# Kernel optimization log

Measured on AMD Instinct MI355X. Metric: run time of the kernel, lower is better.

Reference implementation:

```python
import jax, jax.numpy as jnp
import numpy as np

N = 100_000   # nodes
E = 600_000   # edges
D = 128       # embed_dim
G = 1000      # graphs (batch ids)
L = 3         # num_layers


def setup_inputs() -> dict:
    key = jax.random.key(0)
    ks = jax.random.split(key, 12)
    s = 1.0 / np.sqrt(D)
    return {
        "x": jax.random.normal(ks[0], (N, D), jnp.float32),
        "edge_index": jax.random.randint(ks[1], (2, E), 0, N),
        "batch": jnp.sort(jax.random.randint(ks[2], (N,), 0, G)),
        "mask": jax.random.randint(ks[3], (N,), 0, 2),
        # stacked GCNConv weights/biases (in=hidden=out=D)
        "gcn_w": jax.random.normal(ks[4], (L, D, D), jnp.float32) * s,
        "gcn_b": jnp.zeros((L, D), jnp.float32),
        # MLP head: Linear(D,D) -> ReLU -> Linear(D,1)
        "lin1_w": jax.random.normal(ks[5], (D, D), jnp.float32) * s,
        "lin1_b": jnp.zeros((D,), jnp.float32),
        "lin2_w": jax.random.normal(ks[6], (D,), jnp.float32) * s,
        "lin2_b": jnp.zeros((), jnp.float32),
    }


def gcn_forward(x, src, dst, gcn_w, gcn_b):
    # symmetric gcn_norm with self-loops: deg[i] = 1 + in-degree(i)
    deg = jax.ops.segment_sum(jnp.ones((E,), x.dtype), dst, num_segments=N) + 1.0
    dinv = jax.lax.rsqrt(deg)
    enorm = dinv[src] * dinv[dst]          # [E] edge normalization
    self_norm = (dinv * dinv)[:, None]     # [N,1] self-loop normalization
    h = x
    for l in range(L):
        h = h @ gcn_w[l]                   # [N,D]
        h = (jax.ops.segment_sum(h[src] * enorm[:, None], dst, num_segments=N)
             + h * self_norm)
        h = h + gcn_b[l]
        if l < L - 1:
            h = jax.nn.relu(h)  # (dropout inactive at inference)
    return h


def reference(x, edge_index, batch, mask, gcn_w, gcn_b, lin1_w, lin1_b, lin2_w, lin2_b):
    src, dst = edge_index[0], edge_index[1]
    h = gcn_forward(x, src, dst, gcn_w, gcn_b)
    # MLP head -> per-node score [N]
    s = jax.nn.relu(h @ lin1_w + lin1_b) @ lin2_w + lin2_b
    s = jnp.where(mask == 0, jnp.float32(-1e9), s)
    # per-graph (segment) softmax — fused replacement for the unique/batch loop
    m = jax.ops.segment_max(s, batch, num_segments=G)
    e = jnp.exp(s - m[batch])
    z = jax.ops.segment_sum(e, batch, num_segments=G)
    return e / z[batch]
```

## Files before the change

### kernel.cpp

```cpp
#include <hip/hip_runtime.h>
#include <hip/hip_bf16.h>
#include <stdint.h>

typedef unsigned int u32;
typedef unsigned short u16;
typedef __attribute__((ext_vector_type(8))) short bf16x8;
typedef __attribute__((ext_vector_type(4))) float f32x4;

__device__ __forceinline__ float u16tof(u16 u){ return __uint_as_float(((u32)u) << 16); }
__device__ __forceinline__ float lo16(u32 v){ return __uint_as_float(v << 16); }
__device__ __forceinline__ float hi16(u32 v){ return __uint_as_float(v & 0xffff0000u); }
__device__ __forceinline__ u16 ftobf(float f){
  u32 b = __float_as_uint(f);
  return (u16)((b + 0x7FFFu + ((b >> 16) & 1u)) >> 16);
}
__device__ __forceinline__ u32 pack2(float a, float b){
  return (u32)ftobf(a) | ((u32)ftobf(b) << 16);
}
__device__ __forceinline__ float ldf(const void* p, int i, int isbf){
  return isbf ? u16tof(((const u16*)p)[i]) : ((const float*)p)[i];
}

__device__ __forceinline__ void acc8(float* a, uint4 v, float mk){
  a[0] = fmaf(lo16(v.x), mk, a[0]);
  a[1] = fmaf(hi16(v.x), mk, a[1]);
  a[2] = fmaf(lo16(v.y), mk, a[2]);
  a[3] = fmaf(hi16(v.y), mk, a[3]);
  a[4] = fmaf(lo16(v.z), mk, a[4]);
  a[5] = fmaf(hi16(v.z), mk, a[5]);
  a[6] = fmaf(lo16(v.w), mk, a[6]);
  a[7] = fmaf(hi16(v.w), mk, a[7]);
}

__device__ __forceinline__ void async16(const u16* g, const u16* l){
  __builtin_amdgcn_global_load_lds(
      (const __attribute__((address_space(1))) u32*)(uintptr_t)g,
      (__attribute__((address_space(3))) u32*)(uintptr_t)l,
      16, 0, 0);
}

__global__ __launch_bounds__(256) void k_prep(const void* __restrict__ gw, const void* __restrict__ l1w,
                                              const void* __restrict__ x, u16* __restrict__ Wf,
                                              u16* __restrict__ Hb, int L, int n8, int cvtB, int goffB,
                                              const int* __restrict__ batch, int* __restrict__ goff,
                                              int N, int G,
                                              const int* __restrict__ dst, int* __restrict__ hist,
                                              int nE, int chunk, int* __restrict__ flag){
  __shared__ int sh[256];
  const int b = blockIdx.x;
  const int t = threadIdx.x;
  const int histStart = L + 1 + cvtB + goffB;

  if (b >= histStart){
    sh[t] = 0; __syncthreads();
    const int blk = b - histStart;
    const int e0 = blk * chunk, e1 = min(e0 + chunk, nE);
    for (int e = e0 + t; e < e1; e += 256) atomicAdd(&sh[dst[e] >> 9], 1);
    __syncthreads();
    hist[blk * 256 + t] = sh[t];
    return;
  }
  if (b >= L + 1 + cvtB){
    const int i = (b - (L + 1 + cvtB)) * 256 + t;
    if (i >= N) return;
    const int bt = batch[i];
    const int prev = (i == 0) ? -1 : batch[i - 1];
    for (int g = prev + 1; g <= bt; ++g) goff[g] = i;
    if (i == N - 1){ for (int g = bt + 1; g <= G; ++g) goff[g] = N; }
    return;
  }
  if (t == 0) sh[0] = 0;
  __syncthreads();
  if (b <= L){
    int local = 0;
    for (int i = t; i < 4096; i += 256){
      u32 e = (((const u32*)gw)[i] >> 7) & 0xFFu;
      if (e >= 100u && e < 127u) local++;
    }
    atomicAdd(&sh[0], local);
    __syncthreads();
    const int isbf = (sh[0] > 2048) ? 1 : 0;
    if (b == 0 && t == 0) *flag = isbf;

    const void* src = (b < L) ? gw : l1w;
    const int sbase = (b < L) ? b * 16384 : 0;
    u16* dstp = Wf + (size_t)b * 16384;
    for (int g = t; g < 2048; g += 256){
      const int tt = g >> 8, ks = (g >> 6) & 3, lane = g & 63;
      const int n = tt * 16 + (lane & 15);
      const int k0 = ks * 32 + ((lane >> 4) << 3);
      u16* d = dstp + (size_t)g * 8;
      #pragma unroll
      for (int j = 0; j < 8; ++j){
        d[j] = ftobf(ldf(src, sbase + (k0 + j) * 128 + n, isbf));
      }
    }
  } else {
    u32 e = (((const u32*)gw)[t] >> 7) & 0xFFu;
    atomicAdd(&sh[0], (e >= 100u && e < 127u) ? 1 : 0);
    __syncthreads();
    if (sh[0] > 128) return;
    const int i = (b - (L + 1)) * 256 + t;
    if (i >= n8) return;
    const float4 a = ((const float4*)x)[i * 2];
    const float4 c = ((const float4*)x)[i * 2 + 1];
    u16* o = Hb + (size_t)i * 8;
    o[0] = ftobf(a.x); o[1] = ftobf(a.y); o[2] = ftobf(a.z); o[3] = ftobf(a.w);
    o[4] = ftobf(c.x); o[5] = ftobf(c.y); o[6] = ftobf(c.z); o[7] = ftobf(c.w);
  }
}

__global__ __launch_bounds__(256) void k_hscan(int* __restrict__ hist, int* __restrict__ bb, int nE){
  const int t = threadIdx.x;
  int run = 0;
  for (int j = 0; j < 256; j += 8){
    int v[8];
    #pragma unroll
    for (int k = 0; k < 8; ++k) v[k] = hist[(j + k) * 256 + t];
    #pragma unroll
    for (int k = 0; k < 8; ++k){
      hist[(j + k) * 256 + t] = run;
      run += v[k];
    }
  }
  __shared__ int sm[256];
  sm[t] = run; __syncthreads();
  for (int off = 1; off < 256; off <<= 1){
    int a = (t >= off) ? sm[t - off] : 0;
    __syncthreads();
    sm[t] += a;
    __syncthreads();
  }
  bb[t] = sm[t] - run;
  if (t == 255) bb[256] = nE;
}

__global__ __launch_bounds__(256) void k_scatter(const int* __restrict__ src, const int* __restrict__ dst,
                                                 const int* __restrict__ hist, const int* __restrict__ bb,
                                                 int2* __restrict__ tmpe, int nE, int chunk){
  __shared__ int base[256];
  const int blk = blockIdx.x, t = threadIdx.x;
  base[t] = bb[t] + hist[blk * 256 + t];
  __syncthreads();
  const int e0 = blk * chunk, e1 = min(e0 + chunk, nE);
  for (int e = e0 + t; e < e1; e += 256){
    const int d = dst[e];
    const int pos = atomicAdd(&base[d >> 9], 1);
    tmpe[pos] = make_int2(src[e], d);
  }
}

__global__ __launch_bounds__(256) void k_local(const int2* __restrict__ tmpe, const int* __restrict__ bb,
                                               int* __restrict__ boff, int* __restrict__ eid,
                                               float* __restrict__ dinv, int N, int nE, int nbkt){
  __shared__ int hcnt[512];
  __shared__ int hoff[512];
  const int b = blockIdx.x, t = threadIdx.x;
  const int n0 = b << 9;
  const int n1 = min(n0 + 512, N);
  const int nn = n1 - n0;
  const int e0 = bb[b], e1 = bb[b + 1];
  hcnt[t] = 0; hcnt[t + 256] = 0;
  __syncthreads();
  for (int e = e0 + t; e < e1; e += 256) atomicAdd(&hcnt[tmpe[e].y - n0], 1);
  __syncthreads();
  const int v0 = hcnt[t], v1 = hcnt[t + 256];
  hoff[t] = v0; hoff[t + 256] = v1;
  __syncthreads();
  for (int off = 1; off < 512; off <<= 1){
    int a0 = (t >= off) ? hoff[t - off] : 0;
    int a1 = (t + 256 >= off) ? hoff[t + 256 - off] : 0;
    __syncthreads();
    hoff[t] += a0; hoff[t + 256] += a1;
    __syncthreads();
  }
  const int ex0 = hoff[t] - v0 + e0;
  const int ex1 = hoff[t + 256] - v1 + e0;
  if (t < nn){       boff[n0 + t] = ex0;        dinv[n0 + t] = rsqrtf((float)v0 + 1.0f); }
  if (t + 256 < nn){ boff[n0 + t + 256] = ex1;  dinv[n0 + t + 256] = rsqrtf((float)v1 + 1.0f); }
  if (b == nbkt - 1 && t == 0) boff[N] = nE;
  __syncthreads();
  hoff[t] = ex0; hoff[t + 256] = ex1;
  __syncthreads();
  for (int e = e0 + t; e < e1; e += 256){
    const int2 pr = tmpe[e];
    const int pos = atomicAdd(&hoff[pr.y - n0], 1);
    eid[pos] = pr.x;
  }
}

__global__ __launch_bounds__(256) void k_mm(const void* __restrict__ X, const u16* __restrict__ Hb,
                                            const u16* __restrict__ Wf, const float* __restrict__ dinv,
                                            u16* __restrict__ T, int n, const int* __restrict__ fl){
  __shared__ u16 smw[16384];
  const int isbf = *fl;
  const u16* A = isbf ? (const u16*)X : Hb;
  {
    const uint4* s = (const uint4*)Wf;
    uint4* d = (uint4*)smw;
    for (int i = threadIdx.x; i < 2048; i += 256) d[i] = s[i];
  }
  __syncthreads();

  const int wave = threadIdx.x >> 6, lane = threadIdx.x & 63;
  const int m0 = blockIdx.x * 64 + wave * 16;
  int arow = m0 + (lane & 15); if (arow > n - 1) arow = n - 1;
  const u16* aptr = A + (size_t)arow * 128 + ((lane >> 4) << 3);

  f32x4 acc[8];
  #pragma unroll
  for (int t = 0; t < 8; ++t) acc[t] = (f32x4){0.f, 0.f, 0.f, 0.f};

  #pragma unroll
  for (int ks = 0; ks < 4; ++ks){
    const bf16x8 a = *(const bf16x8*)(aptr + ks * 32);
    #pragma unroll
    for (int t = 0; t < 8; ++t){
      const bf16x8 b = *(const bf16x8*)(smw + (size_t)(((t * 4 + ks) * 64 + lane) * 8));
      acc[t] = __builtin_amdgcn_mfma_f32_16x16x32_bf16(a, b, acc[t], 0, 0, 0);
    }
  }
  __syncthreads();

  const int quad = lane >> 4, col0 = lane & 15;
  float dv[4];
  #pragma unroll
  for (int r = 0; r < 4; ++r){
    const int row = m0 + quad * 4 + r;
    dv[r] = (row < n) ? dinv[row] : 0.f;
  }
  u16* my = smw + wave * 2112;
  #pragma unroll
  for (int t = 0; t < 8; ++t){
    #pragma unroll
    for (int r = 0; r < 4; ++r){
      my[(quad * 4 + r) * 132 + t * 16 + col0] = ftobf(acc[t][r] * dv[r]);
    }
  }
  #pragma unroll
  for (int i = 0; i < 4; ++i){
    const int row = i * 4 + (lane >> 4);
    const int grow = m0 + row;
    const int c8 = (lane & 15) * 8;
    if (grow < n){
      const u16* s = &my[row * 132 + c8];
      uint2 lo = *(const uint2*)(s);
      uint2 hi = *(const uint2*)(s + 4);
      *(uint4*)&T[(size_t)grow * 128 + c8] = make_uint4(lo.x, lo.y, hi.x, hi.y);
    }
  }
}

__global__ __launch_bounds__(256) void k_gath(const u16* __restrict__ Tin, const int* __restrict__ boff,
                                              const int* __restrict__ eid, const float* __restrict__ dinv,
                                              const void* __restrict__ bias, int layer, int dorelu,
                                              u16* __restrict__ Hout, int n, const int* __restrict__ fl){
  __shared__ u16 ring[4][4][512];
  __shared__ int seid[512];
  __shared__ int sboff[17];
  const int isbf = *fl;
  const int tid = threadIdx.x;
  const int wave = tid >> 6, lane = tid & 63;
  const int sub = lane >> 4, l16 = lane & 15;
  const int m0 = blockIdx.x * 16;

  const int e0 = boff[m0];
  const int e1 = boff[min(m0 + 16, n)];
  const int len = e1 - e0;
  const int inlds = (len <= 512);
  if (tid < 17) sboff[tid] = boff[min(m0 + tid, n)];
  if (inlds){ for (int i = tid; i < len; i += 256) seid[i] = eid[e0 + i]; }
  __syncthreads();

  const int wsub = wave * 4 + sub;
  const int node = m0 + wsub;
  const int js = sboff[wsub];
  const int d  = sboff[wsub + 1] - js;

  float a[8];
  #pragma unroll
  for (int k = 0; k < 8; ++k) a[k] = 0.f;
  if (node < n){
    const uint4 sv = ((const uint4*)(Tin + (size_t)node * 128))[l16];
    acc8(a, sv, 1.f);
  }

  int T = 0;
  #pragma unroll
  for (int s2 = 0; s2 < 4; ++s2){
    const int dd = sboff[wave * 4 + s2 + 1] - sboff[wave * 4 + s2];
    T = (dd > T) ? dd : T;
  }

  if (inlds){
    const int jloc = js - e0;
    const int jlast = jloc + ((d > 0) ? (d - 1) : 0);
    const u16* base = Tin + (size_t)l16 * 8;
    u16* slot = &ring[wave][0][0];
    #pragma unroll
    for (int t = 0; t < 4; ++t){
      if (t < T){
        const int idx = (d > 0) ? seid[(t < d) ? (jloc + t) : jlast] : 0;
        async16(base + (size_t)idx * 128, slot + (t & 3) * 512);
      }
    }
    int t = 0;
    for (; t + 4 <= T; ++t){
      asm volatile("s_waitcnt vmcnt(3)" ::: "memory");
      const uint4 v = *(const uint4*)(slot + (t & 3) * 512 + lane * 8);
      acc8(a, v, (t < d) ? 1.f : 0.f);
      const int tn = t + 4;
      if (tn < T){
        const int idx = (d > 0) ? seid[(tn < d) ? (jloc + tn) : jlast] : 0;
        async16(base + (size_t)idx * 128, slot + (tn & 3) * 512);
      }
    }
    for (; t < T; ++t){
      const int rem = T - t - 1;
      if (rem >= 2)      asm volatile("s_waitcnt vmcnt(2)" ::: "memory");
      else if (rem == 1) asm volatile("s_waitcnt vmcnt(1)" ::: "memory");
      else               asm volatile("s_waitcnt vmcnt(0)" ::: "memory");
      const uint4 v = *(const uint4*)(slot + (t & 3) * 512 + lane * 8);
      acc8(a, v, (t < d) ? 1.f : 0.f);
    }
  } else {
    for (int j = js; j < js + d; ++j){
      const uint4 v = ((const uint4*)(Tin + (size_t)eid[j] * 128))[l16];
      acc8(a, v, 1.f);
    }
  }

  if (node < n){
    const float di = dinv[node];
    const int bb = layer * 128 + l16 * 8;
    float h[8];
    #pragma unroll
    for (int k = 0; k < 8; ++k){
      h[k] = fmaf(a[k], di, ldf(bias, bb + k, isbf));
      if (dorelu) h[k] = fmaxf(h[k], 0.f);
    }
    uint4 o;
    o.x = pack2(h[0], h[1]); o.y = pack2(h[2], h[3]); o.z = pack2(h[4], h[5]); o.w = pack2(h[6], h[7]);
    *(uint4*)&Hout[(size_t)node * 128 + l16 * 8] = o;
  }
}

__global__ __launch_bounds__(256) void k_head(const u16* __restrict__ H, const u16* __restrict__ Wf,
                                              const void* __restrict__ b1, const void* __restrict__ w2,
                                              const void* __restrict__ b2, const int* __restrict__ mask,
                                              float* __restrict__ s, int n, const int* __restrict__ fl){
  __shared__ u16 smw[16384];
  __shared__ float sred[4][16];
  const int isbf = *fl;
  {
    const uint4* sp = (const uint4*)Wf;
    uint4* d = (uint4*)smw;
    for (int i = threadIdx.x; i < 2048; i += 256) d[i] = sp[i];
  }
  __syncthreads();

  const int wave = threadIdx.x >> 6, lane = threadIdx.x & 63;
  const int m0 = blockIdx.x * 64 + wave * 16;
  int arow = m0 + (lane & 15); if (arow > n - 1) arow = n - 1;
  const u16* aptr = H + (size_t)arow * 128 + ((lane >> 4) << 3);

  f32x4 acc[8];
  #pragma unroll
  for (int t = 0; t < 8; ++t) acc[t] = (f32x4){0.f, 0.f, 0.f, 0.f};
  #pragma unroll
  for (int ks = 0; ks < 4; ++ks){
    const bf16x8 a = *(const bf16x8*)(aptr + ks * 32);
    #pragma unroll
    for (int t = 0; t < 8; ++t){
      const bf16x8 b = *(const bf16x8*)(smw + (size_t)(((t * 4 + ks) * 64 + lane) * 8));
      acc[t] = __builtin_amdgcn_mfma_f32_16x16x32_bf16(a, b, acc[t], 0, 0, 0);
    }
  }

  const int quad = lane >> 4, col0 = lane & 15;
  float p[4] = {0.f, 0.f, 0.f, 0.f};
  #pragma unroll
  for (int t = 0; t < 8; ++t){
    const int col = t * 16 + col0;
    const float bv = ldf(b1, col, isbf);
    const float wv = ldf(w2, col, isbf);
    #pragma unroll
    for (int r = 0; r < 4; ++r){
      p[r] = fmaf(fmaxf(acc[t][r] + bv, 0.f), wv, p[r]);
    }
  }
  #pragma unroll
  for (int k = 1; k < 16; k <<= 1){
    #pragma unroll
    for (int r = 0; r < 4; ++r) p[r] += __shfl_xor(p[r], k);
  }
  if (col0 == 0){
    #pragma unroll
    for (int r = 0; r < 4; ++r) sred[wave][quad * 4 + r] = p[r];
  }
  __syncthreads();
  if (threadIdx.x < 64){
    const int row = blockIdx.x * 64 + threadIdx.x;
    if (row < n){
      const int w = threadIdx.x >> 4, idx = threadIdx.x & 15;
      float sc = sred[w][idx] + ldf(b2, 0, isbf);
      if (mask[row] == 0) sc = -1e9f;
      s[row] = sc;
    }
  }
}

__global__ __launch_bounds__(256) void k_gsm(const float* __restrict__ s, const int* __restrict__ goff,
                                             void* __restrict__ out, int G, const int* __restrict__ fl){
  const int g = blockIdx.x * 4 + (threadIdx.x >> 6);
  if (g >= G) return;
  const int lane = threadIdx.x & 63;
  const int i0 = goff[g], i1 = goff[g + 1];
  if (i0 >= i1) return;
  float m = -3.4e38f;
  for (int j = i0 + lane; j < i1; j += 64) m = fmaxf(m, s[j]);
  #pragma unroll
  for (int k = 32; k; k >>= 1) m = fmaxf(m, __shfl_xor(m, k));
  float zz = 0.f;
  for (int j = i0 + lane; j < i1; j += 64) zz += expf(s[j] - m);
  #pragma unroll
  for (int k = 32; k; k >>= 1) zz += __shfl_xor(zz, k);
  const float rz = 1.f / zz;
  const int isbf = *fl;
  for (int j = i0 + lane; j < i1; j += 64){
    const float v = expf(s[j] - m) * rz;
    if (isbf) ((u16*)out)[j] = ftobf(v);
    else      ((float*)out)[j] = v;
  }
}

extern "C" void kernel_launch(void* const* d_in, const int* in_sizes, int n_in,
                              void* d_out, int out_size, void* d_ws, size_t ws_size,
                              hipStream_t stream){
  const void* x    = d_in[0];
  const int* ei    = (const int*)d_in[1];
  const int* batch = (const int*)d_in[2];
  const int* mask  = (const int*)d_in[3];
  const void* gw   = d_in[4];
  const void* gb   = d_in[5];
  const void* l1w  = d_in[6];
  const void* l1b  = d_in[7];
  const void* l2w  = d_in[8];
  const void* l2b  = d_in[9];

  const int N = in_sizes[2];
  const int E = in_sizes[1] / 2;
  const int D = 128;
  const int L = in_sizes[4] / (D * D);
  const int G = 1000;

  char* p = (char*)d_ws;
  u16*  Hb    = (u16*)p;   p += (size_t)N * D * sizeof(u16);
  u16*  Tb    = (u16*)p;   p += (size_t)N * D * sizeof(u16);
  u16*  Wf    = (u16*)p;   p += (size_t)(L + 1) * D * D * sizeof(u16);
  float* dinv = (float*)p; p += (size_t)N * sizeof(float);
  float* sbuf = (float*)p; p += (size_t)N * sizeof(float);
  int*  boff  = (int*)p;   p += (size_t)(N + 1) * sizeof(int);
  int*  eid   = (int*)p;   p += (size_t)E * sizeof(int);
  int*  goff  = (int*)p;   p += (size_t)(G + 1) * sizeof(int);
  int*  hist  = (int*)p;   p += 256 * 256 * sizeof(int);
  int*  bb    = (int*)p;   p += 260 * sizeof(int);
  int2* tmpe  = (int2*)p;  p += (size_t)E * sizeof(int2);
  int*  flag  = (int*)p;   p += 256;

  const int* srcp = ei;
  const int* dstp = ei + E;

  const int mmg   = (N + 63) / 64;
  const int fg    = (N + 15) / 16;
  const int n8    = N * D / 8;
  const int cvtB  = (n8 + 255) / 256;
  const int goffB = (N + 255) / 256;
  const int chunk = (E + 255) / 256;
  const int nbkt  = (N + 511) / 512;

  k_prep<<<(L + 1) + cvtB + goffB + 256, 256, 0, stream>>>(gw, l1w, x, Wf, Hb, L, n8, cvtB, goffB,
                                                           batch, goff, N, G, dstp, hist, E, chunk, flag);
  k_hscan<<<1, 256, 0, stream>>>(hist, bb, E);
  k_scatter<<<256, 256, 0, stream>>>(srcp, dstp, hist, bb, tmpe, E, chunk);
  k_local<<<nbkt, 256, 0, stream>>>(tmpe, bb, boff, eid, dinv, N, E, nbkt);

  k_mm<<<mmg, 256, 0, stream>>>(x, Hb, Wf, dinv, Tb, N, flag);
  k_gath<<<fg, 256, 0, stream>>>(Tb, boff, eid, dinv, gb, 0, 1, Hb, N, flag);
  k_mm<<<mmg, 256, 0, stream>>>(Hb, Hb, Wf + (size_t)1 * D * D, dinv, Tb, N, flag);
  k_gath<<<fg, 256, 0, stream>>>(Tb, boff, eid, dinv, gb, 1, 1, Hb, N, flag);
  k_mm<<<mmg, 256, 0, stream>>>(Hb, Hb, Wf + (size_t)2 * D * D, dinv, Tb, N, flag);
  k_gath<<<fg, 256, 0, stream>>>(Tb, boff, eid, dinv, gb, 2, 0, Hb, N, flag);
  k_head<<<mmg, 256, 0, stream>>>(Hb, Wf + (size_t)L * D * D, l1b, l2w, l2b, mask, sbuf, N, flag);
  k_gsm<<<(G + 3) / 4, 256, 0, stream>>>(sbuf, goff, d_out, G, flag);
}
```

Before: 325.8 us.

## Build CSR via global-atomic degree count and scan; fuse fp32 input conversion into GEMM

Replaces the two-level bucketed CSR build (block histograms, bucket scatter to a temp edge array, local sort) with global atomic degree counting, a three-pass exclusive scan, and an atomic fill of edge sources. It also removes the separate fp32-to-bf16 conversion pass over x by converting inside the first GEMM's A-operand load. The aim is fewer passes over edge data and less intermediate traffic. In exchange it relies on heavily contended global atomics and more kernel launches. Neighbour order within each row now depends on atomic timing, so results are not deterministic.

```diff
diff --git a/kernel.cpp b/kernel.cpp
--- a/kernel.cpp
+++ b/kernel.cpp
@@ -39,29 +39,29 @@
       16, 0, 0);
 }
 
+__global__ __launch_bounds__(256) void k_zero(int* __restrict__ deg, int N){
+  const int i = blockIdx.x * 256 + threadIdx.x;
+  if (i < N) deg[i] = 0;
+}
+
 __global__ __launch_bounds__(256) void k_prep(const void* __restrict__ gw, const void* __restrict__ l1w,
-                                              const void* __restrict__ x, u16* __restrict__ Wf,
-                                              u16* __restrict__ Hb, int L, int n8, int cvtB, int goffB,
+                                              u16* __restrict__ Wf, int L, int goffB,
                                               const int* __restrict__ batch, int* __restrict__ goff,
                                               int N, int G,
-                                              const int* __restrict__ dst, int* __restrict__ hist,
+                                              const int* __restrict__ dst, int* __restrict__ deg,
                                               int nE, int chunk, int* __restrict__ flag){
-  __shared__ int sh[256];
+  __shared__ int sh[1];
   const int b = blockIdx.x;
   const int t = threadIdx.x;
-  const int histStart = L + 1 + cvtB + goffB;
-
-  if (b >= histStart){
-    sh[t] = 0; __syncthreads();
-    const int blk = b - histStart;
+
+  if (b >= L + 1 + goffB){
+    const int blk = b - (L + 1 + goffB);
     const int e0 = blk * chunk, e1 = min(e0 + chunk, nE);
-    for (int e = e0 + t; e < e1; e += 256) atomicAdd(&sh[dst[e] >> 9], 1);
-    __syncthreads();
-    hist[blk * 256 + t] = sh[t];
+    for (int e = e0 + t; e < e1; e += 256) atomicAdd(&deg[dst[e]], 1);
     return;
   }
-  if (b >= L + 1 + cvtB){
-    const int i = (b - (L + 1 + cvtB)) * 256 + t;
+  if (b >= L + 1){
+    const int i = (b - (L + 1)) * 256 + t;
     if (i >= N) return;
     const int bt = batch[i];
     const int prev = (i == 0) ? -1 : batch[i - 1];
@@ -71,130 +71,93 @@
   }
   if (t == 0) sh[0] = 0;
   __syncthreads();
-  if (b <= L){
-    int local = 0;
-    for (int i = t; i < 4096; i += 256){
-      u32 e = (((const u32*)gw)[i] >> 7) & 0xFFu;
-      if (e >= 100u && e < 127u) local++;
-    }
-    atomicAdd(&sh[0], local);
-    __syncthreads();
-    const int isbf = (sh[0] > 2048) ? 1 : 0;
-    if (b == 0 && t == 0) *flag = isbf;
-
-    const void* src = (b < L) ? gw : l1w;
-    const int sbase = (b < L) ? b * 16384 : 0;
-    u16* dstp = Wf + (size_t)b * 16384;
-    for (int g = t; g < 2048; g += 256){
-      const int tt = g >> 8, ks = (g >> 6) & 3, lane = g & 63;
-      const int n = tt * 16 + (lane & 15);
-      const int k0 = ks * 32 + ((lane >> 4) << 3);
-      u16* d = dstp + (size_t)g * 8;
-      #pragma unroll
-      for (int j = 0; j < 8; ++j){
-        d[j] = ftobf(ldf(src, sbase + (k0 + j) * 128 + n, isbf));
-      }
-    }
-  } else {
-    u32 e = (((const u32*)gw)[t] >> 7) & 0xFFu;
-    atomicAdd(&sh[0], (e >= 100u && e < 127u) ? 1 : 0);
-    __syncthreads();
-    if (sh[0] > 128) return;
-    const int i = (b - (L + 1)) * 256 + t;
-    if (i >= n8) return;
-    const float4 a = ((const float4*)x)[i * 2];
-    const float4 c = ((const float4*)x)[i * 2 + 1];
-    u16* o = Hb + (size_t)i * 8;
-    o[0] = ftobf(a.x); o[1] = ftobf(a.y); o[2] = ftobf(a.z); o[3] = ftobf(a.w);
-    o[4] = ftobf(c.x); o[5] = ftobf(c.y); o[6] = ftobf(c.z); o[7] = ftobf(c.w);
-  }
-}
-
-__global__ __launch_bounds__(256) void k_hscan(int* __restrict__ hist, int* __restrict__ bb, int nE){
+  int local = 0;
+  for (int i = t; i < 4096; i += 256){
+    u32 e = (((const u32*)gw)[i] >> 7) & 0xFFu;
+    if (e >= 100u && e < 127u) local++;
+  }
+  atomicAdd(&sh[0], local);
+  __syncthreads();
+  const int isbf = (sh[0] > 2048) ? 1 : 0;
+  if (b == 0 && t == 0) *flag = isbf;
+
+  const void* src = (b < L) ? gw : l1w;
+  const int sbase = (b < L) ? b * 16384 : 0;
+  u16* dstp = Wf + (size_t)b * 16384;
+  for (int g = t; g < 2048; g += 256){
+    const int tt = g >> 8, ks = (g >> 6) & 3, lane = g & 63;
+    const int n = tt * 16 + (lane & 15);
+    const int k0 = ks * 32 + ((lane >> 4) << 3);
+    u16* d = dstp + (size_t)g * 8;
+    #pragma unroll
+    for (int j = 0; j < 8; ++j){
+      d[j] = ftobf(ldf(src, sbase + (k0 + j) * 128 + n, isbf));
+    }
+  }
+}
+
+__global__ __launch_bounds__(256) void k_scanA(const int* __restrict__ deg, int* __restrict__ boff,
+                                               int* __restrict__ bsum, int N){
+  __shared__ int sm[256];
   const int t = threadIdx.x;
-  int run = 0;
-  for (int j = 0; j < 256; j += 8){
-    int v[8];
-    #pragma unroll
-    for (int k = 0; k < 8; ++k) v[k] = hist[(j + k) * 256 + t];
-    #pragma unroll
-    for (int k = 0; k < 8; ++k){
-      hist[(j + k) * 256 + t] = run;
-      run += v[k];
-    }
-  }
-  __shared__ int sm[256];
-  sm[t] = run; __syncthreads();
+  const int i = blockIdx.x * 256 + t;
+  const int d = (i < N) ? deg[i] : 0;
+  sm[t] = d; __syncthreads();
   for (int off = 1; off < 256; off <<= 1){
     int a = (t >= off) ? sm[t - off] : 0;
     __syncthreads();
     sm[t] += a;
     __syncthreads();
   }
-  bb[t] = sm[t] - run;
-  if (t == 255) bb[256] = nE;
-}
-
-__global__ __launch_bounds__(256) void k_scatter(const int* __restrict__ src, const int* __restrict__ dst,
-                                                 const int* __restrict__ hist, const int* __restrict__ bb,
-                                                 int2* __restrict__ tmpe, int nE, int chunk){
-  __shared__ int base[256];
+  if (i < N) boff[i] = sm[t] - d;
+  if (t == 255) bsum[blockIdx.x] = sm[255];
+}
+
+__global__ __launch_bounds__(512) void k_scanB(int* __restrict__ bsum, int nblk){
+  __shared__ int sm[512];
+  const int t = threadIdx.x;
+  const int v = (t < nblk) ? bsum[t] : 0;
+  sm[t] = v; __syncthreads();
+  for (int off = 1; off < 512; off <<= 1){
+    int a = (t >= off) ? sm[t - off] : 0;
+    __syncthreads();
+    sm[t] += a;
+    __syncthreads();
+  }
+  if (t < nblk) bsum[t] = sm[t] - v;
+}
+
+__global__ __launch_bounds__(256) void k_scanC(const int* __restrict__ deg, int* __restrict__ boff,
+                                               const int* __restrict__ bsum, int* __restrict__ cur,
+                                               float* __restrict__ dinv, int N, int nE){
+  const int t = threadIdx.x;
+  const int i = blockIdx.x * 256 + t;
+  if (i < N){
+    const int b = boff[i] + bsum[blockIdx.x];
+    boff[i] = b;
+    cur[i] = b;
+    dinv[i] = rsqrtf((float)deg[i] + 1.0f);
+  }
+  if (blockIdx.x == 0 && t == 0) boff[N] = nE;
+}
+
+__global__ __launch_bounds__(256) void k_fill(const int* __restrict__ src, const int* __restrict__ dst,
+                                              int* __restrict__ cur, int* __restrict__ eid,
+                                              int nE, int chunk){
   const int blk = blockIdx.x, t = threadIdx.x;
-  base[t] = bb[t] + hist[blk * 256 + t];
-  __syncthreads();
   const int e0 = blk * chunk, e1 = min(e0 + chunk, nE);
   for (int e = e0 + t; e < e1; e += 256){
-    const int d = dst[e];
-    const int pos = atomicAdd(&base[d >> 9], 1);
-    tmpe[pos] = make_int2(src[e], d);
-  }
-}
-
-__global__ __launch_bounds__(256) void k_local(const int2* __restrict__ tmpe, const int* __restrict__ bb,
-                                               int* __restrict__ boff, int* __restrict__ eid,
-                                               float* __restrict__ dinv, int N, int nE, int nbkt){
-  __shared__ int hcnt[512];
-  __shared__ int hoff[512];
-  const int b = blockIdx.x, t = threadIdx.x;
-  const int n0 = b << 9;
-  const int n1 = min(n0 + 512, N);
-  const int nn = n1 - n0;
-  const int e0 = bb[b], e1 = bb[b + 1];
-  hcnt[t] = 0; hcnt[t + 256] = 0;
-  __syncthreads();
-  for (int e = e0 + t; e < e1; e += 256) atomicAdd(&hcnt[tmpe[e].y - n0], 1);
-  __syncthreads();
-  const int v0 = hcnt[t], v1 = hcnt[t + 256];
-  hoff[t] = v0; hoff[t + 256] = v1;
-  __syncthreads();
-  for (int off = 1; off < 512; off <<= 1){
-    int a0 = (t >= off) ? hoff[t - off] : 0;
-    int a1 = (t + 256 >= off) ? hoff[t + 256 - off] : 0;
-    __syncthreads();
-    hoff[t] += a0; hoff[t + 256] += a1;
-    __syncthreads();
-  }
-  const int ex0 = hoff[t] - v0 + e0;
-  const int ex1 = hoff[t + 256] - v1 + e0;
-  if (t < nn){       boff[n0 + t] = ex0;        dinv[n0 + t] = rsqrtf((float)v0 + 1.0f); }
-  if (t + 256 < nn){ boff[n0 + t + 256] = ex1;  dinv[n0 + t + 256] = rsqrtf((float)v1 + 1.0f); }
-  if (b == nbkt - 1 && t == 0) boff[N] = nE;
-  __syncthreads();
-  hoff[t] = ex0; hoff[t + 256] = ex1;
-  __syncthreads();
-  for (int e = e0 + t; e < e1; e += 256){
-    const int2 pr = tmpe[e];
-    const int pos = atomicAdd(&hoff[pr.y - n0], 1);
-    eid[pos] = pr.x;
-  }
-}
-
-__global__ __launch_bounds__(256) void k_mm(const void* __restrict__ X, const u16* __restrict__ Hb,
-                                            const u16* __restrict__ Wf, const float* __restrict__ dinv,
-                                            u16* __restrict__ T, int n, const int* __restrict__ fl){
+    const int pos = atomicAdd(&cur[dst[e]], 1);
+    eid[pos] = src[e];
+  }
+}
+
+__global__ __launch_bounds__(256) void k_mm(const void* __restrict__ X, const u16* __restrict__ Wf,
+                                            const float* __restrict__ dinv, u16* __restrict__ T,
+                                            int n, int cvtin, const int* __restrict__ fl){
   __shared__ u16 smw[16384];
   const int isbf = *fl;
-  const u16* A = isbf ? (const u16*)X : Hb;
+  const int fp32in = cvtin && !isbf;
   {
     const uint4* s = (const uint4*)Wf;
     uint4* d = (uint4*)smw;
@@ -205,7 +168,7 @@
   const int wave = threadIdx.x >> 6, lane = threadIdx.x & 63;
   const int m0 = blockIdx.x * 64 + wave * 16;
   int arow = m0 + (lane & 15); if (arow > n - 1) arow = n - 1;
-  const u16* aptr = A + (size_t)arow * 128 + ((lane >> 4) << 3);
+  const int koff = (lane >> 4) << 3;
 
   f32x4 acc[8];
   #pragma unroll
@@ -213,7 +176,16 @@
 
   #pragma unroll
   for (int ks = 0; ks < 4; ++ks){
-    const bf16x8 a = *(const bf16x8*)(aptr + ks * 32);
+    bf16x8 a;
+    if (fp32in){
+      const float* ap = (const float*)X + (size_t)arow * 128 + koff + ks * 32;
+      const float4 f0 = *(const float4*)ap;
+      const float4 f1 = *(const float4*)(ap + 4);
+      a = (bf16x8){(short)ftobf(f0.x), (short)ftobf(f0.y), (short)ftobf(f0.z), (short)ftobf(f0.w),
+                   (short)ftobf(f1.x), (short)ftobf(f1.y), (short)ftobf(f1.z), (short)ftobf(f1.w)};
+    } else {
+      a = *(const bf16x8*)((const u16*)X + (size_t)arow * 128 + koff + ks * 32);
+    }
     #pragma unroll
     for (int t = 0; t < 8; ++t){
       const bf16x8 b = *(const bf16x8*)(smw + (size_t)(((t * 4 + ks) * 64 + lane) * 8));
@@ -463,9 +435,9 @@
   int*  boff  = (int*)p;   p += (size_t)(N + 1) * sizeof(int);
   int*  eid   = (int*)p;   p += (size_t)E * sizeof(int);
   int*  goff  = (int*)p;   p += (size_t)(G + 1) * sizeof(int);
-  int*  hist  = (int*)p;   p += 256 * 256 * sizeof(int);
-  int*  bb    = (int*)p;   p += 260 * sizeof(int);
-  int2* tmpe  = (int2*)p;  p += (size_t)E * sizeof(int2);
+  int*  deg   = (int*)p;   p += (size_t)N * sizeof(int);
+  int*  cur   = (int*)p;   p += (size_t)N * sizeof(int);
+  int*  bsum  = (int*)p;   p += 512 * sizeof(int);
   int*  flag  = (int*)p;   p += 256;
 
   const int* srcp = ei;
@@ -473,23 +445,23 @@
 
   const int mmg   = (N + 63) / 64;
   const int fg    = (N + 15) / 16;
-  const int n8    = N * D / 8;
-  const int cvtB  = (n8 + 255) / 256;
   const int goffB = (N + 255) / 256;
+  const int scanG = (N + 255) / 256;
   const int chunk = (E + 255) / 256;
-  const int nbkt  = (N + 511) / 512;
-
-  k_prep<<<(L + 1) + cvtB + goffB + 256, 256, 0, stream>>>(gw, l1w, x, Wf, Hb, L, n8, cvtB, goffB,
-                                                           batch, goff, N, G, dstp, hist, E, chunk, flag);
-  k_hscan<<<1, 256, 0, stream>>>(hist, bb, E);
-  k_scatter<<<256, 256, 0, stream>>>(srcp, dstp, hist, bb, tmpe, E, chunk);
-  k_local<<<nbkt, 256, 0, stream>>>(tmpe, bb, boff, eid, dinv, N, E, nbkt);
-
-  k_mm<<<mmg, 256, 0, stream>>>(x, Hb, Wf, dinv, Tb, N, flag);
+
+  k_zero<<<scanG, 256, 0, stream>>>(deg, N);
+  k_prep<<<(L + 1) + goffB + 256, 256, 0, stream>>>(gw, l1w, Wf, L, goffB,
+                                                    batch, goff, N, G, dstp, deg, E, chunk, flag);
+  k_scanA<<<scanG, 256, 0, stream>>>(deg, boff, bsum, N);
+  k_scanB<<<1, 512, 0, stream>>>(bsum, scanG);
+  k_scanC<<<scanG, 256, 0, stream>>>(deg, boff, bsum, cur, dinv, N, E);
+  k_fill<<<256, 256, 0, stream>>>(srcp, dstp, cur, eid, E, chunk);
+
+  k_mm<<<mmg, 256, 0, stream>>>(x, Wf, dinv, Tb, N, 1, flag);
   k_gath<<<fg, 256, 0, stream>>>(Tb, boff, eid, dinv, gb, 0, 1, Hb, N, flag);
-  k_mm<<<mmg, 256, 0, stream>>>(Hb, Hb, Wf + (size_t)1 * D * D, dinv, Tb, N, flag);
+  k_mm<<<mmg, 256, 0, stream>>>(Hb, Wf + (size_t)1 * D * D, dinv, Tb, N, 0, flag);
   k_gath<<<fg, 256, 0, stream>>>(Tb, boff, eid, dinv, gb, 1, 1, Hb, N, flag);
-  k_mm<<<mmg, 256, 0, stream>>>(Hb, Hb, Wf + (size_t)2 * D * D, dinv, Tb, N, flag);
+  k_mm<<<mmg, 256, 0, stream>>>(Hb, Wf + (size_t)2 * D * D, dinv, Tb, N, 0, flag);
   k_gath<<<fg, 256, 0, stream>>>(Tb, boff, eid, dinv, gb, 2, 0, Hb, N, flag);
   k_head<<<mmg, 256, 0, stream>>>(Hb, Wf + (size_t)L * D * D, l1b, l2w, l2b, mask, sbuf, N, flag);
   k_gsm<<<(G + 3) / 4, 256, 0, stream>>>(sbuf, goff, d_out, G, flag);
```

Result: slower. 354.6 us (+8.8%).
